# Kernel tuning notes

Measured on AMD Instinct MI355X. Metric: run time of the kernel, lower is better.

## Reference

```python
import jax, jax.numpy as jnp
import numpy as np

RADIUS = 4  # matches init_kwargs
EPS = 1e-12  # torch F.normalize eps


def _l2_normalize(x):
    # normalize over channel dim (axis=1), matching F.normalize(p=2, dim=1)
    n = jnp.sqrt(jnp.sum(x * x, axis=1, keepdims=True))
    return x / jnp.maximum(n, EPS)


def setup_inputs() -> dict:
    key = jax.random.key(0)
    k1, k2 = jax.random.split(key)
    B, C, H, W = 8, 256, 128, 192
    return {
        "feat1": jax.random.normal(k1, (B, C, H, W), dtype=jnp.float32),
        "feat2": jax.random.normal(k2, (B, C, H, W), dtype=jnp.float32),
    }


def reference(feat1, feat2):
    r = RADIUS
    B, C, H, W = feat1.shape
    f1 = _l2_normalize(feat1)
    f2 = _l2_normalize(feat2)
    f2p = jnp.pad(f2, ((0, 0), (0, 0), (r, r), (r, r)))  # [B,C,H+2r,W+2r]
    # fixed (2r+1)^2 = 81 static offsets; loop is over offsets, not data dims
    corrs = []
    for dy in range(-r, r + 1):
        for dx in range(-r, r + 1):
            shifted = f2p[:, :, dy + r:dy + r + H, dx + r:dx + r + W]
            corrs.append(jnp.sum(f1 * shifted, axis=1))  # [B,H,W]
    return jnp.stack(corrs, axis=1)  # [B,(2r+1)^2,H,W]
```

## Files before the change

### kernel.cpp

```cpp
#include <hip/hip_runtime.h>
#include <math.h>

namespace {

constexpr int B_ = 8, C_ = 256, H_ = 128, W_ = 192;
constexpr int HW = H_ * W_;
constexpr size_t CHW = (size_t)C_ * HW;
constexpr int TH = 8, TW = 16;
constexpr int NTHREADS = 512;
constexpr int KCH = 16;
constexpr int NCHUNK = C_ / KCH;
constexpr int BROWS = 16;
constexpr int BPOS = 32;
constexpr int POSB = 48;
constexpr int ROWB = BPOS * POSB;
constexpr int BUFB = BROWS * ROWB;
constexpr int LDSB = 2 * BUFB;
constexpr int OSTR = 20;
constexpr int OUTB = 81 * 4 * OSTR * 4;
constexpr int BNOFF = OUTB;

typedef _Float16 f16x4 __attribute__((ext_vector_type(4)));
typedef _Float16 f16x8 __attribute__((ext_vector_type(8)));
typedef float f32x4 __attribute__((ext_vector_type(4)));
typedef _Float16 h2 __attribute__((ext_vector_type(2)));

__device__ __forceinline__ unsigned pk2(float x, float y) {
    return __builtin_bit_cast(unsigned, __builtin_amdgcn_cvt_pkrtz(x, y));
}
__device__ __forceinline__ float dot2f(unsigned a, unsigned b, float c) {
#if __has_builtin(__builtin_amdgcn_fdot2)
    return __builtin_amdgcn_fdot2(__builtin_bit_cast(h2, a),
                                  __builtin_bit_cast(h2, b), c, false);
#else
    const h2 ha = __builtin_bit_cast(h2, a), hb = __builtin_bit_cast(h2, b);
    return fmaf((float)ha.x, (float)hb.x, fmaf((float)ha.y, (float)hb.y, c));
#endif
}
__device__ __forceinline__ f32x4 mfma16(f16x4 a, f16x4 b, f32x4 c) {
#if __has_builtin(__builtin_amdgcn_mfma_f32_16x16x16f16)
    return __builtin_amdgcn_mfma_f32_16x16x16f16(a, b, c, 0, 0, 0);
#else
    const f16x8 a8 = {a[0], a[1], a[2], a[3], (_Float16)0, (_Float16)0, (_Float16)0, (_Float16)0};
    const f16x8 b8 = {b[0], b[1], b[2], b[3], (_Float16)0, (_Float16)0, (_Float16)0, (_Float16)0};
    return __builtin_amdgcn_mfma_f32_16x16x32_f16(a8, b8, c, 0, 0, 0);
#endif
}

__device__ __forceinline__ void publish_barrier() {
    asm volatile("s_waitcnt lgkmcnt(0)" ::: "memory");
    __builtin_amdgcn_sched_barrier(0);
    __builtin_amdgcn_s_barrier();
    __builtin_amdgcn_sched_barrier(0);
}

__global__ __launch_bounds__(NTHREADS)
void local_corr_mfma(const float* __restrict__ f1g,
                     const float* __restrict__ f2g,
                     float* __restrict__ outg)
{
    __shared__ __align__(16) char lds[LDSB];

    const int m  = blockIdx.x;
    const int b  = m & 7;
    const int k  = m >> 3;
    const int bx = k % 12;
    const int by = k / 12;
    const int w0 = bx * TW, h0 = by * TH;

    const int tid  = threadIdx.x;
    const int hs   = tid >> 6;
    const int lane = tid & 63;
    const int lp   = lane & 15;
    const int lg   = lane >> 4;

    const int sr = tid >> 5;
    const int sc = tid & 31;
    const int bgh = h0 - 4 + sr, bgw = w0 - 8 + sc;
    const bool bok = (bgh >= 0) && (bgh < H_) && (bgw >= 0) && (bgw < W_);
    const int bghc = min(max(bgh, 0), H_ - 1);
    const int bgwc = min(max(bgw, 0), W_ - 1);
    const float* bptr = f2g + (size_t)b * CHW + (size_t)bghc * W_ + bgwc;
    const float* aptr = f1g + (size_t)b * CHW + (size_t)(h0 + hs) * W_ + (w0 + lp)
                            + (size_t)(4 * lg) * HW;

    float bvr[16], avr[4];
    float bn = 0.f, an = 0.f;
    f16x4 afrag;

    auto issue = [&]() {
#pragma unroll
        for (int j = 0; j < 16; ++j) bvr[j] = bptr[(size_t)j * HW];
#pragma unroll
        for (int j = 0; j < 4; ++j) avr[j] = aptr[(size_t)j * HW];
        bptr += (size_t)KCH * HW;
        aptr += (size_t)KCH * HW;
    };

    auto stage = [&](int buf) {
        unsigned u[8];
#pragma unroll
        for (int q = 0; q < 8; ++q) {
            const float x = bok ? bvr[2 * q] : 0.f;
            const float y = bok ? bvr[2 * q + 1] : 0.f;
            u[q] = pk2(x, y);
            bn = dot2f(u[q], u[q], bn);
        }
        char* dst = lds + buf * BUFB + tid * POSB;
        *reinterpret_cast<uint4*>(dst)      = make_uint4(u[0], u[1], u[2], u[3]);
        *reinterpret_cast<uint4*>(dst + 16) = make_uint4(u[4], u[5], u[6], u[7]);
        const unsigned a0 = pk2(avr[0], avr[1]);
        const unsigned a1 = pk2(avr[2], avr[3]);
        an = dot2f(a0, a0, an);
        an = dot2f(a1, a1, an);
        afrag = __builtin_bit_cast(f16x4, make_uint2(a0, a1));
    };

    f32x4 acc[9][2];
#pragma unroll
    for (int dy = 0; dy < 9; ++dy)
#pragma unroll
        for (int bt = 0; bt < 2; ++bt) acc[dy][bt] = (f32x4)0.f;

    const int fro = lp * POSB + lg * 8;

    auto compute = [&](int buf) {
        __builtin_amdgcn_s_setprio(1);
#pragma unroll
        for (int dy = 0; dy < 9; ++dy) {
            const char* rbase = lds + buf * BUFB + (hs + dy) * ROWB + fro;
            const f16x4 b0 = *reinterpret_cast<const f16x4*>(rbase);
            const f16x4 b1 = *reinterpret_cast<const f16x4*>(rbase + 16 * POSB);
            acc[dy][0] = mfma16(afrag, b0, acc[dy][0]);
            acc[dy][1] = mfma16(afrag, b1, acc[dy][1]);
        }
        __builtin_amdgcn_s_setprio(0);
    };

    issue();
    stage(0);
    issue();
    publish_barrier();
    for (int t = 0; t < NCHUNK; t += 2) {
        compute(0);
        stage(1);
        if (t + 2 < NCHUNK) issue();
        publish_barrier();
        compute(1);
        if (t + 2 < NCHUNK) {
            stage(0);
            if (t + 3 < NCHUNK) issue();
        }
        publish_barrier();
    }

    float* bnorm = reinterpret_cast<float*>(lds + BNOFF);
    bnorm[tid] = bn;
    an += __shfl_xor(an, 16);
    an += __shfl_xor(an, 32);
    const float inv1own = 1.0f / fmaxf(sqrtf(an), 1e-12f);
    __syncthreads();

    const size_t obase = (size_t)b * 81 * HW;
#pragma unroll
    for (int pass = 0; pass < 2; ++pass) {
        if ((hs >> 2) == pass) {
            const int h4 = hs & 3;
#pragma unroll
            for (int dy = 0; dy < 9; ++dy) {
#pragma unroll
                for (int bt = 0; bt < 2; ++bt) {
                    const int scol = bt * 16 + lp;
                    const float nb = bnorm[(hs + dy) * 32 + scol];
                    const float v2 = 1.0f / fmaxf(sqrtf(nb), 1e-12f);
#pragma unroll
                    for (int r = 0; r < 4; ++r) {
                        const int mw  = 4 * lg + r;
                        const int dxi = scol - 4 - mw;
                        const float v1 = __shfl(inv1own, mw);
                        if (dxi >= 0 && dxi <= 8) {
                            float* orow = reinterpret_cast<float*>(lds)
                                        + ((dy * 9 + dxi) * 4 + h4) * OSTR;
                            orow[mw] = acc[dy][bt][r] * v1 * v2;
                        }
                    }
                }
            }
        }
        __syncthreads();
        for (int s = tid; s < 81 * 4 * 4; s += NTHREADS) {
            const int od = s >> 4;
            const int rem = s & 15;
            const int h4 = rem >> 2, q = rem & 3;
            const float4 v = *reinterpret_cast<const float4*>(
                reinterpret_cast<const float*>(lds) + (od * 4 + h4) * OSTR + q * 4);
            *reinterpret_cast<float4*>(outg + obase + (size_t)od * HW +
                                       (size_t)(h0 + pass * 4 + h4) * W_ + w0 + q * 4) = v;
        }
        if (pass == 0) __syncthreads();
    }
}

}

extern "C" void kernel_launch(void* const* d_in, const int* in_sizes, int n_in,
                              void* d_out, int out_size, void* d_ws, size_t ws_size,
                              hipStream_t stream)
{
    (void)in_sizes; (void)n_in; (void)d_ws; (void)ws_size; (void)out_size;
    const float* f1 = (const float*)d_in[0];
    const float* f2 = (const float*)d_in[1];
    float* out = (float*)d_out;

    dim3 grid(1536, 1, 1);
    dim3 block(NTHREADS);
    local_corr_mfma<<<grid, block, 0, stream>>>(f1, f2, out);
}
```

Measured before the change: 174.0 us.

## Switch to 16x16x32 MFMA with 32-channel superchunks

```diff
diff --git a/kernel.cpp b/kernel.cpp
--- a/kernel.cpp
+++ b/kernel.cpp
@@ -8,11 +8,11 @@
 constexpr size_t CHW = (size_t)C_ * HW;
 constexpr int TH = 8, TW = 16;
 constexpr int NTHREADS = 512;
-constexpr int KCH = 16;
-constexpr int NCHUNK = C_ / KCH;
+constexpr int KSUP = 32;
+constexpr int NSUP = C_ / KSUP;
 constexpr int BROWS = 16;
 constexpr int BPOS = 32;
-constexpr int POSB = 48;
+constexpr int POSB = 80;
 constexpr int ROWB = BPOS * POSB;
 constexpr int BUFB = BROWS * ROWB;
 constexpr int LDSB = 2 * BUFB;
@@ -20,7 +20,6 @@
 constexpr int OUTB = 81 * 4 * OSTR * 4;
 constexpr int BNOFF = OUTB;
 
-typedef _Float16 f16x4 __attribute__((ext_vector_type(4)));
 typedef _Float16 f16x8 __attribute__((ext_vector_type(8)));
 typedef float f32x4 __attribute__((ext_vector_type(4)));
 typedef _Float16 h2 __attribute__((ext_vector_type(2)));
@@ -37,15 +36,6 @@
     return fmaf((float)ha.x, (float)hb.x, fmaf((float)ha.y, (float)hb.y, c));
 #endif
 }
-__device__ __forceinline__ f32x4 mfma16(f16x4 a, f16x4 b, f32x4 c) {
-#if __has_builtin(__builtin_amdgcn_mfma_f32_16x16x16f16)
-    return __builtin_amdgcn_mfma_f32_16x16x16f16(a, b, c, 0, 0, 0);
-#else
-    const f16x8 a8 = {a[0], a[1], a[2], a[3], (_Float16)0, (_Float16)0, (_Float16)0, (_Float16)0};
-    const f16x8 b8 = {b[0], b[1], b[2], b[3], (_Float16)0, (_Float16)0, (_Float16)0, (_Float16)0};
-    return __builtin_amdgcn_mfma_f32_16x16x32_f16(a8, b8, c, 0, 0, 0);
-#endif
-}
 
 __device__ __forceinline__ void publish_barrier() {
     asm volatile("s_waitcnt lgkmcnt(0)" ::: "memory");
@@ -80,24 +70,24 @@
     const bool bok = (bgh >= 0) && (bgh < H_) && (bgw >= 0) && (bgw < W_);
     const int bghc = min(max(bgh, 0), H_ - 1);
     const int bgwc = min(max(bgw, 0), W_ - 1);
-    const float* bptr = f2g + (size_t)b * CHW + (size_t)bghc * W_ + bgwc;
-    const float* aptr = f1g + (size_t)b * CHW + (size_t)(h0 + hs) * W_ + (w0 + lp)
-                            + (size_t)(4 * lg) * HW;
+    const float* bbase = f2g + (size_t)b * CHW + (size_t)bghc * W_ + bgwc;
+    const float* abase = f1g + (size_t)b * CHW + (size_t)(h0 + hs) * W_ + (w0 + lp)
+                             + (size_t)(8 * lg) * HW;
 
     float bvr[16], avr[4];
+    unsigned aw[4];
     float bn = 0.f, an = 0.f;
-    f16x4 afrag;
-
-    auto issue = [&]() {
-#pragma unroll
-        for (int j = 0; j < 16; ++j) bvr[j] = bptr[(size_t)j * HW];
-#pragma unroll
-        for (int j = 0; j < 4; ++j) avr[j] = aptr[(size_t)j * HW];
-        bptr += (size_t)KCH * HW;
-        aptr += (size_t)KCH * HW;
-    };
-
-    auto stage = [&](int buf) {
+
+    auto issueB = [&](int c0) {
+#pragma unroll
+        for (int j = 0; j < 16; ++j) bvr[j] = bbase[(size_t)(c0 + j) * HW];
+    };
+    auto issueA = [&](int c0) {
+#pragma unroll
+        for (int j = 0; j < 4; ++j) avr[j] = abase[(size_t)(c0 + j) * HW];
+    };
+
+    auto stageB = [&](int buf, int h) {
         unsigned u[8];
 #pragma unroll
         for (int q = 0; q < 8; ++q) {
@@ -106,14 +96,15 @@
             u[q] = pk2(x, y);
             bn = dot2f(u[q], u[q], bn);
         }
-        char* dst = lds + buf * BUFB + tid * POSB;
+        char* dst = lds + buf * BUFB + tid * POSB + 32 * h;
         *reinterpret_cast<uint4*>(dst)      = make_uint4(u[0], u[1], u[2], u[3]);
         *reinterpret_cast<uint4*>(dst + 16) = make_uint4(u[4], u[5], u[6], u[7]);
         const unsigned a0 = pk2(avr[0], avr[1]);
         const unsigned a1 = pk2(avr[2], avr[3]);
         an = dot2f(a0, a0, an);
         an = dot2f(a1, a1, an);
-        afrag = __builtin_bit_cast(f16x4, make_uint2(a0, a1));
+        aw[2 * h] = a0;
+        aw[2 * h + 1] = a1;
     };
 
     f32x4 acc[9][2];
@@ -122,34 +113,40 @@
 #pragma unroll
         for (int bt = 0; bt < 2; ++bt) acc[dy][bt] = (f32x4)0.f;
 
-    const int fro = lp * POSB + lg * 8;
+    const int fro = lp * POSB + lg * 16;
 
     auto compute = [&](int buf) {
+        const f16x8 afrag = __builtin_bit_cast(f16x8, make_uint4(aw[0], aw[1], aw[2], aw[3]));
         __builtin_amdgcn_s_setprio(1);
 #pragma unroll
         for (int dy = 0; dy < 9; ++dy) {
             const char* rbase = lds + buf * BUFB + (hs + dy) * ROWB + fro;
-            const f16x4 b0 = *reinterpret_cast<const f16x4*>(rbase);
-            const f16x4 b1 = *reinterpret_cast<const f16x4*>(rbase + 16 * POSB);
-            acc[dy][0] = mfma16(afrag, b0, acc[dy][0]);
-            acc[dy][1] = mfma16(afrag, b1, acc[dy][1]);
+            const f16x8 b0 = *reinterpret_cast<const f16x8*>(rbase);
+            const f16x8 b1 = *reinterpret_cast<const f16x8*>(rbase + 16 * POSB);
+            acc[dy][0] = __builtin_amdgcn_mfma_f32_16x16x32_f16(afrag, b0, acc[dy][0], 0, 0, 0);
+            acc[dy][1] = __builtin_amdgcn_mfma_f32_16x16x32_f16(afrag, b1, acc[dy][1], 0, 0, 0);
         }
         __builtin_amdgcn_s_setprio(0);
     };
 
-    issue();
-    stage(0);
-    issue();
+    issueB(0);  issueA(0);
+    stageB(0, 0);
+    issueB(16); issueA(4);
+    stageB(0, 1);
+    issueB(32); issueA(32);
     publish_barrier();
-    for (int t = 0; t < NCHUNK; t += 2) {
-        compute(0);
-        stage(1);
-        if (t + 2 < NCHUNK) issue();
+    for (int s = 0; s < NSUP; ++s) {
+        const int cur = s & 1, nxt = cur ^ 1;
+        compute(cur);
+        if (s + 1 < NSUP) {
+            stageB(nxt, 0);
+            issueB(32 * (s + 1) + 16);
+            issueA(32 * (s + 1) + 4);
+        }
         publish_barrier();
-        compute(1);
-        if (t + 2 < NCHUNK) {
-            stage(0);
-            if (t + 3 < NCHUNK) issue();
+        if (s + 1 < NSUP) {
+            stageB(nxt, 1);
+            if (s + 2 < NSUP) { issueB(32 * (s + 2)); issueA(32 * (s + 2)); }
         }
         publish_barrier();
     }
@@ -159,6 +156,9 @@
     an += __shfl_xor(an, 16);
     an += __shfl_xor(an, 32);
     const float inv1own = 1.0f / fmaxf(sqrtf(an), 1e-12f);
+    float inv1v[4];
+#pragma unroll
+    for (int r = 0; r < 4; ++r) inv1v[r] = __shfl(inv1own, 4 * lg + r);
     __syncthreads();
 
     const size_t obase = (size_t)b * 81 * HW;
@@ -177,11 +177,10 @@
                     for (int r = 0; r < 4; ++r) {
                         const int mw  = 4 * lg + r;
                         const int dxi = scol - 4 - mw;
-                        const float v1 = __shfl(inv1own, mw);
                         if (dxi >= 0 && dxi <= 8) {
                             float* orow = reinterpret_cast<float*>(lds)
                                         + ((dy * 9 + dxi) * 4 + h4) * OSTR;
-                            orow[mw] = acc[dy][bt][r] * v1 * v2;
+                            orow[mw] = acc[dy][bt][r] * inv1v[r] * v2;
                         }
                     }
                 }
```

New measurement: 199.5 us. +14.7%, slower.

## Shrink f2 halo staging to 24 columns with overlapping MFMA tiles

Applied to the files above, without the earlier changes.

```diff
diff --git a/kernel.cpp b/kernel.cpp
--- a/kernel.cpp
+++ b/kernel.cpp
@@ -11,11 +11,12 @@
 constexpr int KCH = 16;
 constexpr int NCHUNK = C_ / KCH;
 constexpr int BROWS = 16;
-constexpr int BPOS = 32;
+constexpr int BPOS = 24;
 constexpr int POSB = 48;
-constexpr int ROWB = BPOS * POSB;
+constexpr int ROWB = BPOS * POSB + 16;
 constexpr int BUFB = BROWS * ROWB;
 constexpr int LDSB = 2 * BUFB;
+constexpr int NSTG = BROWS * BPOS;
 constexpr int OSTR = 20;
 constexpr int OUTB = 81 * 4 * OSTR * 4;
 constexpr int BNOFF = OUTB;
@@ -74,23 +75,27 @@
     const int lp   = lane & 15;
     const int lg   = lane >> 4;
 
-    const int sr = tid >> 5;
-    const int sc = tid & 31;
-    const int bgh = h0 - 4 + sr, bgw = w0 - 8 + sc;
-    const bool bok = (bgh >= 0) && (bgh < H_) && (bgw >= 0) && (bgw < W_);
+    const bool isStage = tid < NSTG;
+    const int sr = tid / BPOS;
+    const int sp = tid % BPOS;
+    const int bgh = h0 - 4 + sr, bgw = w0 - 4 + sp;
+    const bool bok = isStage && (bgh >= 0) && (bgh < H_) && (bgw >= 0) && (bgw < W_);
     const int bghc = min(max(bgh, 0), H_ - 1);
     const int bgwc = min(max(bgw, 0), W_ - 1);
     const float* bptr = f2g + (size_t)b * CHW + (size_t)bghc * W_ + bgwc;
     const float* aptr = f1g + (size_t)b * CHW + (size_t)(h0 + hs) * W_ + (w0 + lp)
                             + (size_t)(4 * lg) * HW;
+    const int swoff = sr * ROWB + sp * POSB;
 
     float bvr[16], avr[4];
     float bn = 0.f, an = 0.f;
     f16x4 afrag;
 
     auto issue = [&]() {
-#pragma unroll
-        for (int j = 0; j < 16; ++j) bvr[j] = bptr[(size_t)j * HW];
+        if (isStage) {
+#pragma unroll
+            for (int j = 0; j < 16; ++j) bvr[j] = bptr[(size_t)j * HW];
+        }
 #pragma unroll
         for (int j = 0; j < 4; ++j) avr[j] = aptr[(size_t)j * HW];
         bptr += (size_t)KCH * HW;
@@ -98,17 +103,19 @@
     };
 
     auto stage = [&](int buf) {
-        unsigned u[8];
-#pragma unroll
-        for (int q = 0; q < 8; ++q) {
-            const float x = bok ? bvr[2 * q] : 0.f;
-            const float y = bok ? bvr[2 * q + 1] : 0.f;
-            u[q] = pk2(x, y);
-            bn = dot2f(u[q], u[q], bn);
-        }
-        char* dst = lds + buf * BUFB + tid * POSB;
-        *reinterpret_cast<uint4*>(dst)      = make_uint4(u[0], u[1], u[2], u[3]);
-        *reinterpret_cast<uint4*>(dst + 16) = make_uint4(u[4], u[5], u[6], u[7]);
+        if (isStage) {
+            unsigned u[8];
+#pragma unroll
+            for (int q = 0; q < 8; ++q) {
+                const float x = bok ? bvr[2 * q] : 0.f;
+                const float y = bok ? bvr[2 * q + 1] : 0.f;
+                u[q] = pk2(x, y);
+                bn = dot2f(u[q], u[q], bn);
+            }
+            char* dst = lds + buf * BUFB + swoff;
+            *reinterpret_cast<uint4*>(dst)      = make_uint4(u[0], u[1], u[2], u[3]);
+            *reinterpret_cast<uint4*>(dst + 16) = make_uint4(u[4], u[5], u[6], u[7]);
+        }
         const unsigned a0 = pk2(avr[0], avr[1]);
         const unsigned a1 = pk2(avr[2], avr[3]);
         an = dot2f(a0, a0, an);
@@ -130,7 +137,7 @@
         for (int dy = 0; dy < 9; ++dy) {
             const char* rbase = lds + buf * BUFB + (hs + dy) * ROWB + fro;
             const f16x4 b0 = *reinterpret_cast<const f16x4*>(rbase);
-            const f16x4 b1 = *reinterpret_cast<const f16x4*>(rbase + 16 * POSB);
+            const f16x4 b1 = *reinterpret_cast<const f16x4*>(rbase + 8 * POSB);
             acc[dy][0] = mfma16(afrag, b0, acc[dy][0]);
             acc[dy][1] = mfma16(afrag, b1, acc[dy][1]);
         }
@@ -155,12 +162,17 @@
     }
 
     float* bnorm = reinterpret_cast<float*>(lds + BNOFF);
-    bnorm[tid] = bn;
+    if (isStage) bnorm[tid] = bn;
     an += __shfl_xor(an, 16);
     an += __shfl_xor(an, 32);
     const float inv1own = 1.0f / fmaxf(sqrtf(an), 1e-12f);
+    float inv1v[4];
+#pragma unroll
+    for (int r = 0; r < 4; ++r) inv1v[r] = __shfl(inv1own, 4 * lg + r);
     __syncthreads();
 
+    const bool hiTile = lg >= 2;
+    const int pos     = lp + (hiTile ? 8 : 0);
     const size_t obase = (size_t)b * 81 * HW;
 #pragma unroll
     for (int pass = 0; pass < 2; ++pass) {
@@ -168,21 +180,17 @@
             const int h4 = hs & 3;
 #pragma unroll
             for (int dy = 0; dy < 9; ++dy) {
-#pragma unroll
-                for (int bt = 0; bt < 2; ++bt) {
-                    const int scol = bt * 16 + lp;
-                    const float nb = bnorm[(hs + dy) * 32 + scol];
-                    const float v2 = 1.0f / fmaxf(sqrtf(nb), 1e-12f);
-#pragma unroll
-                    for (int r = 0; r < 4; ++r) {
-                        const int mw  = 4 * lg + r;
-                        const int dxi = scol - 4 - mw;
-                        const float v1 = __shfl(inv1own, mw);
-                        if (dxi >= 0 && dxi <= 8) {
-                            float* orow = reinterpret_cast<float*>(lds)
-                                        + ((dy * 9 + dxi) * 4 + h4) * OSTR;
-                            orow[mw] = acc[dy][bt][r] * v1 * v2;
-                        }
+                const float nb = bnorm[(hs + dy) * BPOS + pos];
+                const float v2 = 1.0f / fmaxf(sqrtf(nb), 1e-12f);
+                const f32x4 a4 = hiTile ? acc[dy][1] : acc[dy][0];
+#pragma unroll
+                for (int r = 0; r < 4; ++r) {
+                    const int mw  = 4 * lg + r;
+                    const int dxi = pos - mw;
+                    if (dxi >= 0 && dxi <= 8) {
+                        float* orow = reinterpret_cast<float*>(lds)
+                                    + ((dy * 9 + dxi) * 4 + h4) * OSTR;
+                        orow[mw] = a4[r] * inv1v[r] * v2;
                     }
                 }
             }
```

After: 235.9 us. +35.6%, slower.
